# Optimization experiments

Measured on AMD Instinct MI355X. Metric: run time of the kernel, lower is better.

Reference implementation:

```python
import jax, jax.numpy as jnp
import numpy as np

N, T, D_FEAT, H = 8192, 60, 6, 64
NEG_SLOPE = 0.01  # torch LeakyReLU default


def setup_inputs() -> dict:
    key = jax.random.key(0)
    ks = jax.random.split(key, 20)
    s = lambda k, shape, fan: jax.random.normal(k, shape, jnp.float32) * (1.0 / np.sqrt(fan))
    inp = {
        'x': jax.random.normal(ks[0], (N, T, D_FEAT), jnp.float32),
        # LSTM layer 0 (input D_FEAT) and layer 1 (input H); gate order i,f,g,o
        'Wih0': s(ks[1], (4 * H, D_FEAT), H), 'Whh0': s(ks[2], (4 * H, H), H),
        'bih0': s(ks[3], (4 * H,), H), 'bhh0': s(ks[4], (4 * H,), H),
        'Wih1': s(ks[5], (4 * H, H), H), 'Whh1': s(ks[6], (4 * H, H), H),
        'bih1': s(ks[7], (4 * H,), H), 'bhh1': s(ks[8], (4 * H,), H),
        # GAT layer: transformation Linear(H,H) and attention vector a [2H,1] (randn in torch)
        'Wt': s(ks[9], (H, H), H), 'bt': s(ks[10], (H,), H),
        'a': jax.random.normal(ks[11], (2 * H, 1), jnp.float32),
        # fc and fc_out
        'Wfc': s(ks[12], (H, H), H), 'bfc': s(ks[13], (H,), H),
        'Wout': s(ks[14], (1, H), H), 'bout': s(ks[15], (1,), H),
    }
    return inp


def _lstm_layer(x, Wih, Whh, bih, bhh):
    # x: [N, T, Din] -> outputs [N, T, H]
    xg = jnp.einsum('ntd,gd->ntg', x, Wih) + bih + bhh  # precompute input gates

    def step(carry, xt):
        h, c = carry
        gates = xt + h @ Whh.T  # [N, 4H]
        i, f, g, o = jnp.split(gates, 4, axis=-1)
        c = jax.nn.sigmoid(f) * c + jax.nn.sigmoid(i) * jnp.tanh(g)
        h = jax.nn.sigmoid(o) * jnp.tanh(c)
        return (h, c), h

    n = x.shape[0]
    h0 = jnp.zeros((n, Whh.shape[1]), x.dtype)
    (_, _), hs = jax.lax.scan(step, (h0, h0), jnp.swapaxes(xg, 0, 1))
    return jnp.swapaxes(hs, 0, 1)


def _gat_layer(x, Wt, bt, a):
    # att[i,j] = leaky_relu(a1 . Wx_j + a2 . Wx_i); softmax over j; out = att @ x
    h = x @ Wt.T + bt                    # [N, H]
    hdim = h.shape[1]
    s1 = (h @ a[:hdim]).squeeze(-1)      # a1 . Wx_j  -> column term
    s2 = (h @ a[hdim:]).squeeze(-1)      # a2 . Wx_i  -> row term
    scores = jax.nn.leaky_relu(s2[:, None] + s1[None, :], NEG_SLOPE)  # [N, N]
    att = jax.nn.softmax(scores, axis=1)
    return att @ x


def reference(x, Wih0, Whh0, bih0, bhh0, Wih1, Whh1, bih1, bhh1,
              Wt, bt, a, Wfc, bfc, Wout, bout):
    out = _lstm_layer(x, Wih0, Whh0, bih0, bhh0)
    out = _lstm_layer(out, Wih1, Whh1, bih1, bhh1)
    last = out[:, -1, :]                 # [N, H]
    hidden = _gat_layer(last, Wt, bt, a) + last  # num_layers_gat = 1
    hidden = jax.nn.leaky_relu(hidden @ Wfc.T + bfc, NEG_SLOPE)
    return (hidden @ Wout.T + bout).squeeze(-1)  # [N]
```

## Files before the change

kernel.cpp:

```cpp
#include <hip/hip_runtime.h>

#define NN 8192
#define TT 60
#define DF 6
#define HH 64
#define GG 256
#define RS 132
#define CH 32
#define NB 256

typedef _Float16 half8 __attribute__((ext_vector_type(8)));
typedef float f32x4 __attribute__((ext_vector_type(4)));
#define MFMA16(a, b, c) __builtin_amdgcn_mfma_f32_16x16x32_f16((a), (b), (c), 0, 0, 0)

#define LOG2E 1.44269504f

__device__ __forceinline__ float lrelu_(float x) { return x > 0.0f ? x : 0.01f * x; }

__device__ __forceinline__ float lstm_act2(float gi, float gf, float gg, float go,
                                           float& c)
{
    const float ei = __builtin_amdgcn_exp2f(gi * -LOG2E);
    const float ef = __builtin_amdgcn_exp2f(gf * -LOG2E);
    const float eg = __builtin_amdgcn_exp2f(fminf(gg * (-2.f * LOG2E), 63.f));
    const float sf = __builtin_amdgcn_rcpf(1.f + ef);
    const float tg_si = (1.f - eg) * __builtin_amdgcn_rcpf((1.f + ei) * (1.f + eg));
    c = __builtin_fmaf(sf, c, tg_si);
    const float eo = __builtin_amdgcn_exp2f(go * -LOG2E);
    const float ec = __builtin_amdgcn_exp2f(fminf(c * (-2.f * LOG2E), 63.f));
    return (1.f - ec) * __builtin_amdgcn_rcpf((1.f + eo) * (1.f + ec));
}

__device__ __forceinline__ half8 ldw8(const float* __restrict__ p) {
    const float4* q = (const float4*)p;
    float4 u = q[0], v = q[1];
    half8 r;
    r[0]=(_Float16)u.x; r[1]=(_Float16)u.y; r[2]=(_Float16)u.z; r[3]=(_Float16)u.w;
    r[4]=(_Float16)v.x; r[5]=(_Float16)v.y; r[6]=(_Float16)v.z; r[7]=(_Float16)v.w;
    return r;
}

#define SXW (TT * 8 + 8)

__global__ __launch_bounds__(512, 4)
void lstm_fused_kernel(const float* __restrict__ x,
                       const float* __restrict__ Wih0, const float* __restrict__ Whh0,
                       const float* __restrict__ bih0, const float* __restrict__ bhh0,
                       const float* __restrict__ Wih1, const float* __restrict__ Whh1,
                       const float* __restrict__ bih1, const float* __restrict__ bhh1,
                       const float* __restrict__ Wt, const float* __restrict__ bt,
                       const float* __restrict__ av,
                       float* __restrict__ last_out,
                       float* __restrict__ s1g, float* __restrict__ s2g)
{
    __shared__ _Float16 sxp[16][SXW];
    __shared__ _Float16 h0buf[2][16][72];
    __shared__ _Float16 h1buf[2][16][72];
    __shared__ _Float16 zero16[8];
    __shared__ float sv1[HH], sv2[HH], sc12[2];

    const int tid  = threadIdx.x;
    const int w    = tid >> 6;
    const int grp  = w >> 2;
    const int cg   = w & 3;
    const int lane = tid & 63;
    const int quad = lane >> 4;
    const int l15  = lane & 15;
    const int hc   = cg * 16 + l15;
    const int n0   = blockIdx.x * 16;

    for (int i = tid; i < 16 * SXW / 2; i += 512) ((unsigned*)sxp)[i] = 0u;
    for (int i = tid; i < 2 * 16 * 72 / 2; i += 512) ((unsigned*)h0buf)[i] = 0u;
    for (int i = tid; i < 2 * 16 * 72 / 2; i += 512) ((unsigned*)h1buf)[i] = 0u;
    if (tid < 4) ((unsigned*)zero16)[tid] = 0u;
    __syncthreads();

    for (int idx = tid; idx < 16 * TT * DF; idx += 512) {
        const int m = idx / (TT * DF);
        const int r = idx - m * (TT * DF);
        const int t = r / DF;
        const int d = r - t * DF;
        sxp[m][t * 8 + d] = (_Float16)x[(size_t)(n0 + m) * (TT * DF) + r];
    }

    if (tid < HH) {
        float a1 = 0.f, a2 = 0.f;
        #pragma unroll 8
        for (int h = 0; h < HH; h++) {
            const float wt = Wt[h * HH + tid];
            a1 += wt * av[h];
            a2 += wt * av[HH + h];
        }
        sv1[tid] = a1; sv2[tid] = a2;
    } else if (tid == 64 || tid == 65) {
        const float* ap = av + (tid - 64) * HH;
        float c = 0.f;
        #pragma unroll 8
        for (int h = 0; h < HH; h++) c += bt[h] * ap[h];
        sc12[tid - 64] = c;
    }

    half8 wA[4][2], wB[4][2];
    float bias[4];
    half8 hzero;
    #pragma unroll
    for (int j = 0; j < 8; j++) hzero[j] = (_Float16)0.f;

    if (grp == 0) {
        #pragma unroll
        for (int nt = 0; nt < 4; nt++) {
            const int g = nt * 64 + hc;
            wA[nt][0] = ldw8(Whh0 + (size_t)g * HH + quad * 8);
            wA[nt][1] = ldw8(Whh0 + (size_t)g * HH + 32 + quad * 8);
            bias[nt]  = bih0[g] + bhh0[g];
            half8 t = hzero;
            if (quad == 0) {
                #pragma unroll
                for (int j = 0; j < DF; j++) t[j] = (_Float16)Wih0[g * DF + j];
            }
            wB[nt][0] = t;
            wB[nt][1] = hzero;
        }
    } else {
        #pragma unroll
        for (int nt = 0; nt < 4; nt++) {
            const int g = nt * 64 + hc;
            wA[nt][0] = ldw8(Wih1 + (size_t)g * HH + quad * 8);
            wA[nt][1] = ldw8(Wih1 + (size_t)g * HH + 32 + quad * 8);
            wB[nt][0] = ldw8(Whh1 + (size_t)g * HH + quad * 8);
            wB[nt][1] = ldw8(Whh1 + (size_t)g * HH + 32 + quad * 8);
            bias[nt]  = bih1[g] + bhh1[g];
        }
    }

    float cs[4] = {0.f, 0.f, 0.f, 0.f};
    __syncthreads();

    for (int i = 0; i <= TT; i++) {
        const int p = i & 1;
        if (grp == 0) {
            if (i < TT) {
                const half8 a0 = *(const half8*)&h0buf[p][l15][quad * 8];
                const half8 a1 = *(const half8*)&h0buf[p][l15][32 + quad * 8];
                const _Float16* xap = (quad == 0) ? &sxp[l15][i * 8] : zero16;
                const half8 ax = *(const half8*)xap;
                f32x4 gv[4];
                #pragma unroll
                for (int nt = 0; nt < 4; nt++) {
                    f32x4 c; c[0] = bias[nt]; c[1] = bias[nt]; c[2] = bias[nt]; c[3] = bias[nt];
                    c = MFMA16(ax, wB[nt][0], c);
                    c = MFMA16(a0, wA[nt][0], c);
                    c = MFMA16(a1, wA[nt][1], c);
                    gv[nt] = c;
                }
                _Float16 (*h0w)[72] = h0buf[p ^ 1];
                #pragma unroll
                for (int reg = 0; reg < 4; reg++) {
                    const float hv = lstm_act2(gv[0][reg], gv[1][reg], gv[2][reg], gv[3][reg], cs[reg]);
                    h0w[quad * 4 + reg][hc] = (_Float16)hv;
                }
            }
        } else {
            if (i > 0) {
                const half8 a00 = *(const half8*)&h0buf[p][l15][quad * 8];
                const half8 a01 = *(const half8*)&h0buf[p][l15][32 + quad * 8];
                const half8 a10 = *(const half8*)&h1buf[p][l15][quad * 8];
                const half8 a11 = *(const half8*)&h1buf[p][l15][32 + quad * 8];
                f32x4 gv[4];
                #pragma unroll
                for (int nt = 0; nt < 4; nt++) {
                    f32x4 c; c[0] = bias[nt]; c[1] = bias[nt]; c[2] = bias[nt]; c[3] = bias[nt];
                    c = MFMA16(a00, wA[nt][0], c);
                    c = MFMA16(a01, wA[nt][1], c);
                    c = MFMA16(a10, wB[nt][0], c);
                    c = MFMA16(a11, wB[nt][1], c);
                    gv[nt] = c;
                }
                _Float16 (*h1w)[72] = h1buf[p ^ 1];
                #pragma unroll
                for (int reg = 0; reg < 4; reg++) {
                    const float hv = lstm_act2(gv[0][reg], gv[1][reg], gv[2][reg], gv[3][reg], cs[reg]);
                    h1w[quad * 4 + reg][hc] = (_Float16)hv;
                    if (i == TT) last_out[(size_t)(n0 + quad * 4 + reg) * HH + hc] = hv;
                }
            }
        }
        __syncthreads();
    }

    {
        const _Float16 (*hf)[72] = h1buf[1];
        const int r  = tid >> 5;
        const int c0 = tid & 31;
        const float h1a = (float)hf[r][c0];
        const float h1b = (float)hf[r][c0 + 32];
        float p1 = h1a * sv1[c0] + h1b * sv1[c0 + 32];
        float p2 = h1a * sv2[c0] + h1b * sv2[c0 + 32];
        #pragma unroll
        for (int off = 16; off > 0; off >>= 1) {
            p1 += __shfl_xor(p1, off);
            p2 += __shfl_xor(p2, off);
        }
        if (c0 == 0) {
            s1g[n0 + r] = p1 + sc12[0];
            s2g[n0 + r] = p2 + sc12[1];
        }
    }
}

__global__ __launch_bounds__(256)
void rankfac_kernel(const float* __restrict__ s1g, const float* __restrict__ s2g,
                    float* __restrict__ Z, float* __restrict__ Ai, float* __restrict__ Bi,
                    float* __restrict__ U, float* __restrict__ W,
                    int* __restrict__ iperm, float* __restrict__ sortedD)
{
    __shared__ float sb[NN];
    __shared__ float sred[256];
    __shared__ int   sRank[32];
    const int tid = threadIdx.x;
    const int b   = blockIdx.x;
    const int j0  = b * 32;

    for (int idx = tid; idx < NN; idx += 256) sb[idx] = s1g[idx];
    if (tid < 32) sRank[tid] = 0;
    __syncthreads();

    float m = -1e30f;
    for (int idx = tid; idx < NN; idx += 256) m = fmaxf(m, sb[idx]);
    sred[tid] = m;
    __syncthreads();
    for (int s = 128; s > 0; s >>= 1) {
        if (tid < s) sred[tid] = fmaxf(sred[tid], sred[tid + s]);
        __syncthreads();
    }
    const float s1max = sred[0];

    if (tid < 32) {
        const int j = j0 + tid;
        const float z  = s2g[j] + s1max;
        const float mi = lrelu_(z);
        Z[j]  = z;
        Ai[j] = __expf(z - mi);
        Bi[j] = __expf(0.01f * z - mi);
        const float d = sb[j] - s1max;
        U[j] = __expf(d);
        W[j] = __expf(0.01f * d);
    }
    {
        const int jl = tid & 31;
        const int part = tid >> 5;
        const float sj = sb[j0 + jl];
        const int jg = j0 + jl;
        int cnt = 0;
        const int k0 = part * (NN / 8);
        #pragma unroll 4
        for (int k = k0; k < k0 + NN / 8; k++) {
            const float sk = sb[k];
            cnt += (sk < sj || (sk == sj && k < jg)) ? 1 : 0;
        }
        atomicAdd(&sRank[jl], cnt);
    }
    __syncthreads();
    if (tid < 32) {
        const int r = sRank[tid];
        iperm[r] = j0 + tid;
        sortedD[r] = sb[j0 + tid] - s1max;
    }
}

__global__ __launch_bounds__(256)
void scanA_kernel(const float* __restrict__ last, const float* __restrict__ U,
                  const float* __restrict__ W, const int* __restrict__ iperm,
                  float* __restrict__ chunkSum)
{
    __shared__ int   sj[CH];
    __shared__ float su[CH], sw[CH];
    __shared__ float al[CH][HH], bl[CH][HH];
    const int tid = threadIdx.x;
    const int b   = blockIdx.x;
    if (tid < CH) {
        const int j = iperm[b * CH + tid];
        sj[tid] = j; su[tid] = U[j]; sw[tid] = W[j];
    }
    __syncthreads();
    for (int idx = tid; idx < CH * HH; idx += 256) {
        const int rr = idx >> 6, c = idx & 63;
        const float lv = last[(size_t)sj[rr] * HH + c];
        al[rr][c] = su[rr] * lv;
        bl[rr][c] = sw[rr] * lv;
    }
    __syncthreads();
    if (tid < 130) {
        const int c = tid;
        float s = 0.f;
        if (c < 64) {
            for (int rr = 0; rr < CH; rr++) s += al[rr][c];
        } else if (c < 128) {
            for (int rr = 0; rr < CH; rr++) s += bl[rr][c - 64];
        } else if (c == 128) {
            for (int rr = 0; rr < CH; rr++) s += su[rr];
        } else {
            for (int rr = 0; rr < CH; rr++) s += sw[rr];
        }
        chunkSum[b * RS + c] = s;
    }
}

__global__ __launch_bounds__(256)
void scanB_kernel(const float* __restrict__ chunkSum, float* __restrict__ chunkOfs)
{
    __shared__ float wt[4];
    const int c   = blockIdx.x;
    const bool rev = (c < 64) || (c == 128);
    const int tid = threadIdx.x;
    const int lane = tid & 63, wv = tid >> 6;
    const int idx = rev ? (NB - 1 - tid) : tid;
    const float orig = chunkSum[idx * RS + c];
    float v = orig;
    #pragma unroll
    for (int d = 1; d < 64; d <<= 1) {
        const float t = __shfl_up(v, d);
        if (lane >= d) v += t;
    }
    if (lane == 63) wt[wv] = v;
    __syncthreads();
    float off = 0.f;
    for (int q = 0; q < wv; q++) off += wt[q];
    chunkOfs[idx * RS + c] = v + off - orig;
}

__global__ __launch_bounds__(256)
void scanC_kernel(const float* __restrict__ last, const float* __restrict__ U,
                  const float* __restrict__ W, const int* __restrict__ iperm,
                  const float* __restrict__ chunkOfs, float* __restrict__ PP)
{
    __shared__ int   sj[CH];
    __shared__ float su[CH], sw[CH];
    __shared__ float al[CH][HH], bl[CH][HH];
    const int tid = threadIdx.x;
    const int b   = blockIdx.x;
    if (tid < CH) {
        const int j = iperm[b * CH + tid];
        sj[tid] = j; su[tid] = U[j]; sw[tid] = W[j];
    }
    __syncthreads();
    for (int idx = tid; idx < CH * HH; idx += 256) {
        const int rr = idx >> 6, c = idx & 63;
        const float lv = last[(size_t)sj[rr] * HH + c];
        al[rr][c] = su[rr] * lv;
        bl[rr][c] = sw[rr] * lv;
    }
    __syncthreads();
    if (tid < 130) {
        const int c = tid;
        const bool rev = (c < 64) || (c == 128);
        float run = chunkOfs[b * RS + c];
        if (rev) {
            if (b == NB - 1) PP[(size_t)NN * RS + c] = 0.f;
            for (int rr = CH - 1; rr >= 0; rr--) {
                const float val = (c < 64) ? al[rr][c] : su[rr];
                run += val;
                PP[(size_t)(b * CH + rr) * RS + c] = run;
            }
        } else {
            for (int rr = 0; rr < CH; rr++) {
                PP[(size_t)(b * CH + rr) * RS + c] = run;
                run += (c < 128) ? bl[rr][c - 64] : sw[rr];
            }
            if (b == NB - 1) PP[(size_t)NN * RS + c] = run;
        }
    }
}

__global__ __launch_bounds__(256)
void applyfc_kernel(const float* __restrict__ last,
                    const float* __restrict__ Z, const float* __restrict__ Ai, const float* __restrict__ Bi,
                    const float* __restrict__ sortedD, const float* __restrict__ PP,
                    const float* __restrict__ Wfc, const float* __restrict__ bfc,
                    const float* __restrict__ Wout, const float* __restrict__ bout,
                    float* __restrict__ out)
{
    __shared__ float sdD[NN];
    __shared__ float sW[HH][HH + 1];
    __shared__ float sbF[HH], saF[HH];
    const int tid = threadIdx.x;
    for (int idx = tid; idx < NN; idx += 256) sdD[idx] = sortedD[idx];
    for (int idx = tid; idx < HH * HH; idx += 256) {
        const int h = idx >> 6, d = idx & 63;
        sW[d][h] = Wfc[idx];
    }
    if (tid < HH) { sbF[tid] = bfc[tid]; saF[tid] = Wout[tid]; }
    __syncthreads();

    const int wv = tid >> 6, lane = tid & 63;
    const int i0 = blockIdx.x * 32 + wv * 8;
    float zi[8]; int lo[8], hi[8];
    #pragma unroll
    for (int q = 0; q < 8; q++) { zi[q] = Z[i0 + q]; lo[q] = 0; hi[q] = NN; }
    for (int iter = 0; iter < 13; iter++) {
        #pragma unroll
        for (int q = 0; q < 8; q++) {
            if (lo[q] < hi[q]) {
                const int mid = (lo[q] + hi[q]) >> 1;
                const float dm = sdD[mid];
                if (zi[q] + dm > 0.f) hi[q] = mid; else lo[q] = mid + 1;
            }
        }
    }
    float gv[8];
    #pragma unroll
    for (int q = 0; q < 8; q++) {
        const int i = i0 + q;
        const float* rowp = PP + (size_t)lo[q] * RS;
        const float pu  = rowp[lane];
        const float pw  = rowp[64 + lane];
        const float pud = rowp[128];
        const float pwd = rowp[129];
        const float ai = Ai[i], bi = Bi[i];
        const float numer = bi * pw + ai * pu;
        const float den   = bi * pwd + ai * pud;
        const float lv = last[(size_t)i * HH + lane];
        gv[q] = numer * __builtin_amdgcn_rcpf(den) + lv;
    }
    const float bo = bout[0];
    #pragma unroll
    for (int q = 0; q < 8; q++) {
        float acc = sbF[lane];
        #pragma unroll
        for (int d = 0; d < HH; d++) acc += __shfl(gv[q], d) * sW[d][lane];
        float prod = lrelu_(acc) * saF[lane];
        #pragma unroll
        for (int off = 32; off > 0; off >>= 1) prod += __shfl_xor(prod, off);
        if (lane == 0) out[i0 + q] = prod + bo;
    }
}

extern "C" void kernel_launch(void* const* d_in, const int* in_sizes, int n_in,
                              void* d_out, int out_size, void* d_ws, size_t ws_size,
                              hipStream_t stream)
{
    (void)in_sizes; (void)n_in; (void)out_size; (void)ws_size;
    const float* x    = (const float*)d_in[0];
    const float* Wih0 = (const float*)d_in[1];
    const float* Whh0 = (const float*)d_in[2];
    const float* bih0 = (const float*)d_in[3];
    const float* bhh0 = (const float*)d_in[4];
    const float* Wih1 = (const float*)d_in[5];
    const float* Whh1 = (const float*)d_in[6];
    const float* bih1 = (const float*)d_in[7];
    const float* bhh1 = (const float*)d_in[8];
    const float* Wt   = (const float*)d_in[9];
    const float* bt   = (const float*)d_in[10];
    const float* a    = (const float*)d_in[11];
    const float* Wfc  = (const float*)d_in[12];
    const float* bfc  = (const float*)d_in[13];
    const float* Wout = (const float*)d_in[14];
    const float* bout = (const float*)d_in[15];
    float* out = (float*)d_out;

    float* ws       = (float*)d_ws;
    float* last     = ws;
    float* s1g      = last + (size_t)NN*HH;
    float* s2g      = s1g + NN;
    float* Z        = s2g + NN;
    float* Ai       = Z + NN;
    float* Bi       = Ai + NN;
    float* U        = Bi + NN;
    float* W        = U + NN;
    float* sortedD  = W + NN;
    int*   iperm    = (int*)(sortedD + NN);
    float* chunkSum = (float*)(iperm + NN);
    float* chunkOfs = chunkSum + NB*RS;
    float* PP       = chunkOfs + NB*RS;

    lstm_fused_kernel<<<dim3(NN / 16), dim3(512), 0, stream>>>(
        x, Wih0, Whh0, bih0, bhh0, Wih1, Whh1, bih1, bhh1,
        Wt, bt, a, last, s1g, s2g);
    rankfac_kernel<<<dim3(NB), dim3(256), 0, stream>>>(
        s1g, s2g, Z, Ai, Bi, U, W, iperm, sortedD);
    scanA_kernel<<<dim3(NB), dim3(256), 0, stream>>>(last, U, W, iperm, chunkSum);
    scanB_kernel<<<dim3(130), dim3(256), 0, stream>>>(chunkSum, chunkOfs);
    scanC_kernel<<<dim3(NB), dim3(256), 0, stream>>>(last, U, W, iperm, chunkOfs, PP);
    applyfc_kernel<<<dim3(NB), dim3(256), 0, stream>>>(
        last, Z, Ai, Bi, sortedD, PP, Wfc, bfc, Wout, bout, out);
}
```

Before: 258.9 us.

## Split LSTM gate work across 16 waves with LDS gate exchange

The fused LSTM kernel doubles its block size to 1024 threads. Each wave now computes two of the four gate tiles per layer and writes the gate pre-activations to a shared-memory buffer. After a barrier, all threads apply the activations, each handling two sequence rows, so the transcendental work is spread over twice as many lanes. The cost is an extra __syncthreads per timestep, LDS round-trips for the gate values and a larger shared-memory footprint, with fewer resident blocks per CU in exchange for more waves per block.

```diff
diff --git a/kernel.cpp b/kernel.cpp
--- a/kernel.cpp
+++ b/kernel.cpp
@@ -10,6 +10,7 @@
 #define NB 256
 
 typedef _Float16 half8 __attribute__((ext_vector_type(8)));
+typedef _Float16 half2v __attribute__((ext_vector_type(2)));
 typedef float f32x4 __attribute__((ext_vector_type(4)));
 #define MFMA16(a, b, c) __builtin_amdgcn_mfma_f32_16x16x32_f16((a), (b), (c), 0, 0, 0)
 
@@ -42,7 +43,7 @@
 
 #define SXW (TT * 8 + 8)
 
-__global__ __launch_bounds__(512, 4)
+__global__ __launch_bounds__(1024, 8)
 void lstm_fused_kernel(const float* __restrict__ x,
                        const float* __restrict__ Wih0, const float* __restrict__ Whh0,
                        const float* __restrict__ bih0, const float* __restrict__ bhh0,
@@ -56,26 +57,32 @@
     __shared__ _Float16 sxp[16][SXW];
     __shared__ _Float16 h0buf[2][16][72];
     __shared__ _Float16 h1buf[2][16][72];
+    __shared__ float    gbuf[2][16][65][4];
     __shared__ _Float16 zero16[8];
     __shared__ float sv1[HH], sv2[HH], sc12[2];
 
     const int tid  = threadIdx.x;
     const int w    = tid >> 6;
-    const int grp  = w >> 2;
-    const int cg   = w & 3;
+    const int lyr  = w >> 3;
+    const int sub  = w & 7;
+    const int cg   = sub >> 1;
+    const int gh   = sub & 1;
     const int lane = tid & 63;
     const int quad = lane >> 4;
     const int l15  = lane & 15;
     const int hc   = cg * 16 + l15;
     const int n0   = blockIdx.x * 16;
-
-    for (int i = tid; i < 16 * SXW / 2; i += 512) ((unsigned*)sxp)[i] = 0u;
-    for (int i = tid; i < 2 * 16 * 72 / 2; i += 512) ((unsigned*)h0buf)[i] = 0u;
-    for (int i = tid; i < 2 * 16 * 72 / 2; i += 512) ((unsigned*)h1buf)[i] = 0u;
+    const int seqA0 = sub;
+    const int seqA1 = sub + 8;
+    const int colA  = lane;
+
+    for (int i = tid; i < 16 * SXW / 2; i += 1024) ((unsigned*)sxp)[i] = 0u;
+    for (int i = tid; i < 2 * 16 * 72 / 2; i += 1024) ((unsigned*)h0buf)[i] = 0u;
+    for (int i = tid; i < 2 * 16 * 72 / 2; i += 1024) ((unsigned*)h1buf)[i] = 0u;
     if (tid < 4) ((unsigned*)zero16)[tid] = 0u;
     __syncthreads();
 
-    for (int idx = tid; idx < 16 * TT * DF; idx += 512) {
+    for (int idx = tid; idx < 16 * TT * DF; idx += 1024) {
         const int m = idx / (TT * DF);
         const int r = idx - m * (TT * DF);
         const int t = r / DF;
@@ -100,95 +107,108 @@
         sc12[tid - 64] = c;
     }
 
-    half8 wA[4][2], wB[4][2];
-    float bias[4];
+    half8 wA[2][2], wB[2][2];
+    float bias[2];
     half8 hzero;
     #pragma unroll
     for (int j = 0; j < 8; j++) hzero[j] = (_Float16)0.f;
 
-    if (grp == 0) {
+    if (lyr == 0) {
         #pragma unroll
-        for (int nt = 0; nt < 4; nt++) {
-            const int g = nt * 64 + hc;
-            wA[nt][0] = ldw8(Whh0 + (size_t)g * HH + quad * 8);
-            wA[nt][1] = ldw8(Whh0 + (size_t)g * HH + 32 + quad * 8);
-            bias[nt]  = bih0[g] + bhh0[g];
+        for (int ln = 0; ln < 2; ln++) {
+            const int g = (gh * 2 + ln) * 64 + hc;
+            wA[ln][0] = ldw8(Whh0 + (size_t)g * HH + quad * 8);
+            wA[ln][1] = ldw8(Whh0 + (size_t)g * HH + 32 + quad * 8);
+            bias[ln]  = bih0[g] + bhh0[g];
             half8 t = hzero;
             if (quad == 0) {
                 #pragma unroll
                 for (int j = 0; j < DF; j++) t[j] = (_Float16)Wih0[g * DF + j];
             }
-            wB[nt][0] = t;
-            wB[nt][1] = hzero;
+            wB[ln][0] = t;
+            wB[ln][1] = hzero;
         }
     } else {
         #pragma unroll
-        for (int nt = 0; nt < 4; nt++) {
-            const int g = nt * 64 + hc;
-            wA[nt][0] = ldw8(Wih1 + (size_t)g * HH + quad * 8);
-            wA[nt][1] = ldw8(Wih1 + (size_t)g * HH + 32 + quad * 8);
-            wB[nt][0] = ldw8(Whh1 + (size_t)g * HH + quad * 8);
-            wB[nt][1] = ldw8(Whh1 + (size_t)g * HH + 32 + quad * 8);
-            bias[nt]  = bih1[g] + bhh1[g];
-        }
-    }
-
-    float cs[4] = {0.f, 0.f, 0.f, 0.f};
+        for (int ln = 0; ln < 2; ln++) {
+            const int g = (gh * 2 + ln) * 64 + hc;
+            wA[ln][0] = ldw8(Wih1 + (size_t)g * HH + quad * 8);
+            wA[ln][1] = ldw8(Wih1 + (size_t)g * HH + 32 + quad * 8);
+            wB[ln][0] = ldw8(Whh1 + (size_t)g * HH + quad * 8);
+            wB[ln][1] = ldw8(Whh1 + (size_t)g * HH + 32 + quad * 8);
+            bias[ln]  = bih1[g] + bhh1[g];
+        }
+    }
+
+    float cs0 = 0.f, cs1 = 0.f;
     __syncthreads();
 
     for (int i = 0; i <= TT; i++) {
         const int p = i & 1;
-        if (grp == 0) {
-            if (i < TT) {
+        const bool live = (lyr == 0) ? (i < TT) : (i > 0);
+
+        if (live) {
+            f32x4 gv0, gv1;
+            if (lyr == 0) {
                 const half8 a0 = *(const half8*)&h0buf[p][l15][quad * 8];
                 const half8 a1 = *(const half8*)&h0buf[p][l15][32 + quad * 8];
                 const _Float16* xap = (quad == 0) ? &sxp[l15][i * 8] : zero16;
                 const half8 ax = *(const half8*)xap;
-                f32x4 gv[4];
-                #pragma unroll
-                for (int nt = 0; nt < 4; nt++) {
-                    f32x4 c; c[0] = bias[nt]; c[1] = bias[nt]; c[2] = bias[nt]; c[3] = bias[nt];
-                    c = MFMA16(ax, wB[nt][0], c);
-                    c = MFMA16(a0, wA[nt][0], c);
-                    c = MFMA16(a1, wA[nt][1], c);
-                    gv[nt] = c;
-                }
-                _Float16 (*h0w)[72] = h0buf[p ^ 1];
-                #pragma unroll
-                for (int reg = 0; reg < 4; reg++) {
-                    const float hv = lstm_act2(gv[0][reg], gv[1][reg], gv[2][reg], gv[3][reg], cs[reg]);
-                    h0w[quad * 4 + reg][hc] = (_Float16)hv;
-                }
-            }
-        } else {
-            if (i > 0) {
+                f32x4 c0; c0[0] = bias[0]; c0[1] = bias[0]; c0[2] = bias[0]; c0[3] = bias[0];
+                c0 = MFMA16(ax, wB[0][0], c0);
+                c0 = MFMA16(a0, wA[0][0], c0);
+                c0 = MFMA16(a1, wA[0][1], c0);
+                f32x4 c1; c1[0] = bias[1]; c1[1] = bias[1]; c1[2] = bias[1]; c1[3] = bias[1];
+                c1 = MFMA16(ax, wB[1][0], c1);
+                c1 = MFMA16(a0, wA[1][0], c1);
+                c1 = MFMA16(a1, wA[1][1], c1);
+                gv0 = c0; gv1 = c1;
+            } else {
                 const half8 a00 = *(const half8*)&h0buf[p][l15][quad * 8];
                 const half8 a01 = *(const half8*)&h0buf[p][l15][32 + quad * 8];
                 const half8 a10 = *(const half8*)&h1buf[p][l15][quad * 8];
                 const half8 a11 = *(const half8*)&h1buf[p][l15][32 + quad * 8];
-                f32x4 gv[4];
-                #pragma unroll
-                for (int nt = 0; nt < 4; nt++) {
-                    f32x4 c; c[0] = bias[nt]; c[1] = bias[nt]; c[2] = bias[nt]; c[3] = bias[nt];
-                    c = MFMA16(a00, wA[nt][0], c);
-                    c = MFMA16(a01, wA[nt][1], c);
-                    c = MFMA16(a10, wB[nt][0], c);
-                    c = MFMA16(a11, wB[nt][1], c);
-                    gv[nt] = c;
+                f32x4 c0; c0[0] = bias[0]; c0[1] = bias[0]; c0[2] = bias[0]; c0[3] = bias[0];
+                c0 = MFMA16(a00, wA[0][0], c0);
+                c0 = MFMA16(a01, wA[0][1], c0);
+                c0 = MFMA16(a10, wB[0][0], c0);
+                c0 = MFMA16(a11, wB[0][1], c0);
+                f32x4 c1; c1[0] = bias[1]; c1[1] = bias[1]; c1[2] = bias[1]; c1[3] = bias[1];
+                c1 = MFMA16(a00, wA[1][0], c1);
+                c1 = MFMA16(a01, wA[1][1], c1);
+                c1 = MFMA16(a10, wB[1][0], c1);
+                c1 = MFMA16(a11, wB[1][1], c1);
+                gv0 = c0; gv1 = c1;
+            }
+            #pragma unroll
+            for (int reg = 0; reg < 4; reg++) {
+                float2 t; t.x = gv0[reg]; t.y = gv1[reg];
+                *(float2*)&gbuf[lyr][quad * 4 + reg][hc][gh * 2] = t;
+            }
+        }
+        __syncthreads();
+
+        if (live) {
+            const float4 g0 = *(const float4*)&gbuf[lyr][seqA0][colA][0];
+            const float4 g1 = *(const float4*)&gbuf[lyr][seqA1][colA][0];
+            const float hv0 = lstm_act2(g0.x, g0.y, g0.z, g0.w, cs0);
+            const float hv1 = lstm_act2(g1.x, g1.y, g1.z, g1.w, cs1);
+            if (lyr == 0) {
+                h0buf[p ^ 1][seqA0][colA] = (_Float16)hv0;
+                h0buf[p ^ 1][seqA1][colA] = (_Float16)hv1;
+            } else {
+                h1buf[p ^ 1][seqA0][colA] = (_Float16)hv0;
+                h1buf[p ^ 1][seqA1][colA] = (_Float16)hv1;
+                if (i == TT) {
+                    last_out[(size_t)(n0 + seqA0) * HH + colA] = hv0;
+                    last_out[(size_t)(n0 + seqA1) * HH + colA] = hv1;
                 }
-                _Float16 (*h1w)[72] = h1buf[p ^ 1];
-                #pragma unroll
-                for (int reg = 0; reg < 4; reg++) {
-                    const float hv = lstm_act2(gv[0][reg], gv[1][reg], gv[2][reg], gv[3][reg], cs[reg]);
-                    h1w[quad * 4 + reg][hc] = (_Float16)hv;
-                    if (i == TT) last_out[(size_t)(n0 + quad * 4 + reg) * HH + hc] = hv;
-                }
             }
         }
         __syncthreads();
     }
 
-    {
+    if (tid < 512) {
         const _Float16 (*hf)[72] = h1buf[1];
         const int r  = tid >> 5;
         const int c0 = tid & 31;
@@ -473,7 +493,7 @@
     float* chunkOfs = chunkSum + NB*RS;
     float* PP       = chunkOfs + NB*RS;
 
-    lstm_fused_kernel<<<dim3(NN / 16), dim3(512), 0, stream>>>(
+    lstm_fused_kernel<<<dim3(NN / 16), dim3(1024), 0, stream>>>(
         x, Wih0, Whh0, bih0, bhh0, Wih1, Whh1, bih1, bhh1,
         Wt, bt, a, last, s1g, s2g);
     rankfac_kernel<<<dim3(NB), dim3(256), 0, stream>>>(
```

Measured after the change: 292.4 us. 13.0% more time.

## Fuse post-LSTM kernels into one cooperative kernel with grid syncs

Applied to the files above, without the earlier changes.

Merges the rank/factor, scan-A, scan-B, scan-C and apply-fc kernels into a single cooperative kernel that uses grid.sync between phases. This removes four kernel launches and their inter-kernel gaps. The separate chunk-offset scan kernel is dropped: each block now sums all preceding or following chunk sums serially, which is redundant O(NB) work per column. Cooperative launch needs all 256 blocks resident at once, and the merged shared-memory footprint is larger.

```diff
diff --git a/kernel.cpp b/kernel.cpp
--- a/kernel.cpp
+++ b/kernel.cpp
@@ -1,4 +1,7 @@
 #include <hip/hip_runtime.h>
+#include <hip/hip_cooperative_groups.h>
+
+namespace cg = cooperative_groups;
 
 #define NN 8192
 #define TT 60
@@ -209,14 +212,27 @@
 }
 
 __global__ __launch_bounds__(256)
-void rankfac_kernel(const float* __restrict__ s1g, const float* __restrict__ s2g,
-                    float* __restrict__ Z, float* __restrict__ Ai, float* __restrict__ Bi,
-                    float* __restrict__ U, float* __restrict__ W,
-                    int* __restrict__ iperm, float* __restrict__ sortedD)
+void post_kernel(const float* __restrict__ last,
+                 const float* __restrict__ s1g, const float* __restrict__ s2g,
+                 float* __restrict__ Z, float* __restrict__ Ai, float* __restrict__ Bi,
+                 float* __restrict__ U, float* __restrict__ W,
+                 int* __restrict__ iperm, float* __restrict__ sortedD,
+                 float* __restrict__ chunkSum, float* __restrict__ PP,
+                 const float* __restrict__ Wfc, const float* __restrict__ bfc,
+                 const float* __restrict__ Wout, const float* __restrict__ bout,
+                 float* __restrict__ out)
 {
+    cg::grid_group grid = cg::this_grid();
+
     __shared__ float sb[NN];
     __shared__ float sred[256];
     __shared__ int   sRank[32];
+    __shared__ int   sj[CH];
+    __shared__ float su[CH], sw[CH];
+    __shared__ float al[CH][HH], bl[CH][HH];
+    __shared__ float sW[HH][HH + 1];
+    __shared__ float sbF[HH], saF[HH];
+
     const int tid = threadIdx.x;
     const int b   = blockIdx.x;
     const int j0  = b * 32;
@@ -249,14 +265,14 @@
     {
         const int jl = tid & 31;
         const int part = tid >> 5;
-        const float sj = sb[j0 + jl];
+        const float sj_ = sb[j0 + jl];
         const int jg = j0 + jl;
         int cnt = 0;
         const int k0 = part * (NN / 8);
         #pragma unroll 4
         for (int k = k0; k < k0 + NN / 8; k++) {
             const float sk = sb[k];
-            cnt += (sk < sj || (sk == sj && k < jg)) ? 1 : 0;
+            cnt += (sk < sj_ || (sk == sj_ && k < jg)) ? 1 : 0;
         }
         atomicAdd(&sRank[jl], cnt);
     }
@@ -266,18 +282,9 @@
         iperm[r] = j0 + tid;
         sortedD[r] = sb[j0 + tid] - s1max;
     }
-}
-
-__global__ __launch_bounds__(256)
-void scanA_kernel(const float* __restrict__ last, const float* __restrict__ U,
-                  const float* __restrict__ W, const int* __restrict__ iperm,
-                  float* __restrict__ chunkSum)
-{
-    __shared__ int   sj[CH];
-    __shared__ float su[CH], sw[CH];
-    __shared__ float al[CH][HH], bl[CH][HH];
-    const int tid = threadIdx.x;
-    const int b   = blockIdx.x;
+
+    grid.sync();
+
     if (tid < CH) {
         const int j = iperm[b * CH + tid];
         sj[tid] = j; su[tid] = U[j]; sw[tid] = W[j];
@@ -304,58 +311,15 @@
         }
         chunkSum[b * RS + c] = s;
     }
-}
-
-__global__ __launch_bounds__(256)
-void scanB_kernel(const float* __restrict__ chunkSum, float* __restrict__ chunkOfs)
-{
-    __shared__ float wt[4];
-    const int c   = blockIdx.x;
-    const bool rev = (c < 64) || (c == 128);
-    const int tid = threadIdx.x;
-    const int lane = tid & 63, wv = tid >> 6;
-    const int idx = rev ? (NB - 1 - tid) : tid;
-    const float orig = chunkSum[idx * RS + c];
-    float v = orig;
-    #pragma unroll
-    for (int d = 1; d < 64; d <<= 1) {
-        const float t = __shfl_up(v, d);
-        if (lane >= d) v += t;
-    }
-    if (lane == 63) wt[wv] = v;
-    __syncthreads();
-    float off = 0.f;
-    for (int q = 0; q < wv; q++) off += wt[q];
-    chunkOfs[idx * RS + c] = v + off - orig;
-}
-
-__global__ __launch_bounds__(256)
-void scanC_kernel(const float* __restrict__ last, const float* __restrict__ U,
-                  const float* __restrict__ W, const int* __restrict__ iperm,
-                  const float* __restrict__ chunkOfs, float* __restrict__ PP)
-{
-    __shared__ int   sj[CH];
-    __shared__ float su[CH], sw[CH];
-    __shared__ float al[CH][HH], bl[CH][HH];
-    const int tid = threadIdx.x;
-    const int b   = blockIdx.x;
-    if (tid < CH) {
-        const int j = iperm[b * CH + tid];
-        sj[tid] = j; su[tid] = U[j]; sw[tid] = W[j];
-    }
-    __syncthreads();
-    for (int idx = tid; idx < CH * HH; idx += 256) {
-        const int rr = idx >> 6, c = idx & 63;
-        const float lv = last[(size_t)sj[rr] * HH + c];
-        al[rr][c] = su[rr] * lv;
-        bl[rr][c] = sw[rr] * lv;
-    }
-    __syncthreads();
+
+    grid.sync();
+
     if (tid < 130) {
         const int c = tid;
         const bool rev = (c < 64) || (c == 128);
-        float run = chunkOfs[b * RS + c];
+        float run = 0.f;
         if (rev) {
+            for (int k = NB - 1; k > b; k--) run += chunkSum[k * RS + c];
             if (b == NB - 1) PP[(size_t)NN * RS + c] = 0.f;
             for (int rr = CH - 1; rr >= 0; rr--) {
                 const float val = (c < 64) ? al[rr][c] : su[rr];
@@ -363,6 +327,7 @@
                 PP[(size_t)(b * CH + rr) * RS + c] = run;
             }
         } else {
+            for (int k = 0; k < b; k++) run += chunkSum[k * RS + c];
             for (int rr = 0; rr < CH; rr++) {
                 PP[(size_t)(b * CH + rr) * RS + c] = run;
                 run += (c < 128) ? bl[rr][c - 64] : sw[rr];
@@ -370,21 +335,10 @@
             if (b == NB - 1) PP[(size_t)NN * RS + c] = run;
         }
     }
-}
-
-__global__ __launch_bounds__(256)
-void applyfc_kernel(const float* __restrict__ last,
-                    const float* __restrict__ Z, const float* __restrict__ Ai, const float* __restrict__ Bi,
-                    const float* __restrict__ sortedD, const float* __restrict__ PP,
-                    const float* __restrict__ Wfc, const float* __restrict__ bfc,
-                    const float* __restrict__ Wout, const float* __restrict__ bout,
-                    float* __restrict__ out)
-{
-    __shared__ float sdD[NN];
-    __shared__ float sW[HH][HH + 1];
-    __shared__ float sbF[HH], saF[HH];
-    const int tid = threadIdx.x;
-    for (int idx = tid; idx < NN; idx += 256) sdD[idx] = sortedD[idx];
+
+    grid.sync();
+
+    for (int idx = tid; idx < NN; idx += 256) sb[idx] = sortedD[idx];
     for (int idx = tid; idx < HH * HH; idx += 256) {
         const int h = idx >> 6, d = idx & 63;
         sW[d][h] = Wfc[idx];
@@ -393,7 +347,7 @@
     __syncthreads();
 
     const int wv = tid >> 6, lane = tid & 63;
-    const int i0 = blockIdx.x * 32 + wv * 8;
+    const int i0 = b * 32 + wv * 8;
     float zi[8]; int lo[8], hi[8];
     #pragma unroll
     for (int q = 0; q < 8; q++) { zi[q] = Z[i0 + q]; lo[q] = 0; hi[q] = NN; }
@@ -402,7 +356,7 @@
         for (int q = 0; q < 8; q++) {
             if (lo[q] < hi[q]) {
                 const int mid = (lo[q] + hi[q]) >> 1;
-                const float dm = sdD[mid];
+                const float dm = sb[mid];
                 if (zi[q] + dm > 0.f) hi[q] = mid; else lo[q] = mid + 1;
             }
         }
@@ -476,11 +430,13 @@
     lstm_fused_kernel<<<dim3(NN / 16), dim3(512), 0, stream>>>(
         x, Wih0, Whh0, bih0, bhh0, Wih1, Whh1, bih1, bhh1,
         Wt, bt, a, last, s1g, s2g);
-    rankfac_kernel<<<dim3(NB), dim3(256), 0, stream>>>(
-        s1g, s2g, Z, Ai, Bi, U, W, iperm, sortedD);
-    scanA_kernel<<<dim3(NB), dim3(256), 0, stream>>>(last, U, W, iperm, chunkSum);
-    scanB_kernel<<<dim3(130), dim3(256), 0, stream>>>(chunkSum, chunkOfs);
-    scanC_kernel<<<dim3(NB), dim3(256), 0, stream>>>(last, U, W, iperm, chunkOfs, PP);
-    applyfc_kernel<<<dim3(NB), dim3(256), 0, stream>>>(
-        last, Z, Ai, Bi, sortedD, PP, Wfc, bfc, Wout, bout, out);
+
+    void* args[] = {
+        (void*)&last, (void*)&s1g, (void*)&s2g,
+        (void*)&Z, (void*)&Ai, (void*)&Bi, (void*)&U, (void*)&W,
+        (void*)&iperm, (void*)&sortedD, (void*)&chunkSum, (void*)&PP,
+        (void*)&Wfc, (void*)&bfc, (void*)&Wout, (void*)&bout, (void*)&out
+    };
+    hipLaunchCooperativeKernel(reinterpret_cast<void*>(post_kernel),
+                               dim3(NB), dim3(256), args, 0, stream);
 }
```

Result: slower. 414.5 us (+60.1%).

## Widen rank/apply blocks, drop scanB by recomputing chunk offsets in scanC

Applied to the files above, without the earlier changes.

The rank kernel now runs 1024 threads per block, uses a wave-shuffle max reduction and float4 LDS reads in the rank-counting loop. The separate scanB launch is removed: each scanC thread sums the other chunks' totals directly, which trades one launch and a sync point for redundant global reads. applyfc now uses 512 threads with 4 rows per wave instead of 8, giving more parallelism for the binary search and FC stage. The LSTM kernel still dominates total time, so the tail-stage gains may be small.

```diff
diff --git a/kernel.cpp b/kernel.cpp
--- a/kernel.cpp
+++ b/kernel.cpp
@@ -208,32 +208,39 @@
     }
 }
 
-__global__ __launch_bounds__(256)
+__global__ __launch_bounds__(1024)
 void rankfac_kernel(const float* __restrict__ s1g, const float* __restrict__ s2g,
                     float* __restrict__ Z, float* __restrict__ Ai, float* __restrict__ Bi,
                     float* __restrict__ U, float* __restrict__ W,
                     int* __restrict__ iperm, float* __restrict__ sortedD)
 {
     __shared__ float sb[NN];
-    __shared__ float sred[256];
+    __shared__ float sredw[16];
     __shared__ int   sRank[32];
-    const int tid = threadIdx.x;
-    const int b   = blockIdx.x;
-    const int j0  = b * 32;
-
-    for (int idx = tid; idx < NN; idx += 256) sb[idx] = s1g[idx];
+    const int tid  = threadIdx.x;
+    const int lane = tid & 63;
+    const int wv   = tid >> 6;
+    const int b    = blockIdx.x;
+    const int j0   = b * 32;
+
+    for (int idx = tid; idx < NN; idx += 1024) sb[idx] = s1g[idx];
     if (tid < 32) sRank[tid] = 0;
     __syncthreads();
 
     float m = -1e30f;
-    for (int idx = tid; idx < NN; idx += 256) m = fmaxf(m, sb[idx]);
-    sred[tid] = m;
-    __syncthreads();
-    for (int s = 128; s > 0; s >>= 1) {
-        if (tid < s) sred[tid] = fmaxf(sred[tid], sred[tid + s]);
-        __syncthreads();
-    }
-    const float s1max = sred[0];
+    for (int idx = tid; idx < NN; idx += 1024) m = fmaxf(m, sb[idx]);
+    #pragma unroll
+    for (int off = 32; off > 0; off >>= 1) m = fmaxf(m, __shfl_xor(m, off));
+    if (lane == 0) sredw[wv] = m;
+    __syncthreads();
+    if (tid == 0) {
+        float mm = sredw[0];
+        #pragma unroll
+        for (int q = 1; q < 16; q++) mm = fmaxf(mm, sredw[q]);
+        sredw[0] = mm;
+    }
+    __syncthreads();
+    const float s1max = sredw[0];
 
     if (tid < 32) {
         const int j = j0 + tid;
@@ -251,12 +258,17 @@
         const int part = tid >> 5;
         const float sj = sb[j0 + jl];
         const int jg = j0 + jl;
+        const int k0 = part * (NN / 32);
+        const float4* sb4 = (const float4*)&sb[k0];
         int cnt = 0;
-        const int k0 = part * (NN / 8);
-        #pragma unroll 4
-        for (int k = k0; k < k0 + NN / 8; k++) {
-            const float sk = sb[k];
-            cnt += (sk < sj || (sk == sj && k < jg)) ? 1 : 0;
+        #pragma unroll 8
+        for (int it = 0; it < NN / 32 / 4; it++) {
+            const float4 v = sb4[it];
+            const int kb = k0 + it * 4;
+            cnt += (v.x < sj || (v.x == sj && kb + 0 < jg)) ? 1 : 0;
+            cnt += (v.y < sj || (v.y == sj && kb + 1 < jg)) ? 1 : 0;
+            cnt += (v.z < sj || (v.z == sj && kb + 2 < jg)) ? 1 : 0;
+            cnt += (v.w < sj || (v.w == sj && kb + 3 < jg)) ? 1 : 0;
         }
         atomicAdd(&sRank[jl], cnt);
     }
@@ -307,32 +319,9 @@
 }
 
 __global__ __launch_bounds__(256)
-void scanB_kernel(const float* __restrict__ chunkSum, float* __restrict__ chunkOfs)
-{
-    __shared__ float wt[4];
-    const int c   = blockIdx.x;
-    const bool rev = (c < 64) || (c == 128);
-    const int tid = threadIdx.x;
-    const int lane = tid & 63, wv = tid >> 6;
-    const int idx = rev ? (NB - 1 - tid) : tid;
-    const float orig = chunkSum[idx * RS + c];
-    float v = orig;
-    #pragma unroll
-    for (int d = 1; d < 64; d <<= 1) {
-        const float t = __shfl_up(v, d);
-        if (lane >= d) v += t;
-    }
-    if (lane == 63) wt[wv] = v;
-    __syncthreads();
-    float off = 0.f;
-    for (int q = 0; q < wv; q++) off += wt[q];
-    chunkOfs[idx * RS + c] = v + off - orig;
-}
-
-__global__ __launch_bounds__(256)
 void scanC_kernel(const float* __restrict__ last, const float* __restrict__ U,
                   const float* __restrict__ W, const int* __restrict__ iperm,
-                  const float* __restrict__ chunkOfs, float* __restrict__ PP)
+                  const float* __restrict__ chunkSum, float* __restrict__ PP)
 {
     __shared__ int   sj[CH];
     __shared__ float su[CH], sw[CH];
@@ -354,8 +343,11 @@
     if (tid < 130) {
         const int c = tid;
         const bool rev = (c < 64) || (c == 128);
-        float run = chunkOfs[b * RS + c];
+        float run = 0.f;
         if (rev) {
+            #pragma unroll 8
+            for (int k = 0; k < NB; k++)
+                run += (k > b) ? chunkSum[k * RS + c] : 0.f;
             if (b == NB - 1) PP[(size_t)NN * RS + c] = 0.f;
             for (int rr = CH - 1; rr >= 0; rr--) {
                 const float val = (c < 64) ? al[rr][c] : su[rr];
@@ -363,6 +355,9 @@
                 PP[(size_t)(b * CH + rr) * RS + c] = run;
             }
         } else {
+            #pragma unroll 8
+            for (int k = 0; k < NB; k++)
+                run += (k < b) ? chunkSum[k * RS + c] : 0.f;
             for (int rr = 0; rr < CH; rr++) {
                 PP[(size_t)(b * CH + rr) * RS + c] = run;
                 run += (c < 128) ? bl[rr][c - 64] : sw[rr];
@@ -372,7 +367,7 @@
     }
 }
 
-__global__ __launch_bounds__(256)
+__global__ __launch_bounds__(512)
 void applyfc_kernel(const float* __restrict__ last,
                     const float* __restrict__ Z, const float* __restrict__ Ai, const float* __restrict__ Bi,
                     const float* __restrict__ sortedD, const float* __restrict__ PP,
@@ -384,8 +379,8 @@
     __shared__ float sW[HH][HH + 1];
     __shared__ float sbF[HH], saF[HH];
     const int tid = threadIdx.x;
-    for (int idx = tid; idx < NN; idx += 256) sdD[idx] = sortedD[idx];
-    for (int idx = tid; idx < HH * HH; idx += 256) {
+    for (int idx = tid; idx < NN; idx += 512) sdD[idx] = sortedD[idx];
+    for (int idx = tid; idx < HH * HH; idx += 512) {
         const int h = idx >> 6, d = idx & 63;
         sW[d][h] = Wfc[idx];
     }
@@ -393,13 +388,13 @@
     __syncthreads();
 
     const int wv = tid >> 6, lane = tid & 63;
-    const int i0 = blockIdx.x * 32 + wv * 8;
-    float zi[8]; int lo[8], hi[8];
+    const int i0 = blockIdx.x * 32 + wv * 4;
+    float zi[4]; int lo[4], hi[4];
     #pragma unroll
-    for (int q = 0; q < 8; q++) { zi[q] = Z[i0 + q]; lo[q] = 0; hi[q] = NN; }
+    for (int q = 0; q < 4; q++) { zi[q] = Z[i0 + q]; lo[q] = 0; hi[q] = NN; }
     for (int iter = 0; iter < 13; iter++) {
         #pragma unroll
-        for (int q = 0; q < 8; q++) {
+        for (int q = 0; q < 4; q++) {
             if (lo[q] < hi[q]) {
                 const int mid = (lo[q] + hi[q]) >> 1;
                 const float dm = sdD[mid];
@@ -407,9 +402,9 @@
             }
         }
     }
-    float gv[8];
+    float gv[4];
     #pragma unroll
-    for (int q = 0; q < 8; q++) {
+    for (int q = 0; q < 4; q++) {
         const int i = i0 + q;
         const float* rowp = PP + (size_t)lo[q] * RS;
         const float pu  = rowp[lane];
@@ -424,7 +419,7 @@
     }
     const float bo = bout[0];
     #pragma unroll
-    for (int q = 0; q < 8; q++) {
+    for (int q = 0; q < 4; q++) {
         float acc = sbF[lane];
         #pragma unroll
         for (int d = 0; d < HH; d++) acc += __shfl(gv[q], d) * sW[d][lane];
@@ -476,11 +471,10 @@
     lstm_fused_kernel<<<dim3(NN / 16), dim3(512), 0, stream>>>(
         x, Wih0, Whh0, bih0, bhh0, Wih1, Whh1, bih1, bhh1,
         Wt, bt, a, last, s1g, s2g);
-    rankfac_kernel<<<dim3(NB), dim3(256), 0, stream>>>(
+    rankfac_kernel<<<dim3(NB), dim3(1024), 0, stream>>>(
         s1g, s2g, Z, Ai, Bi, U, W, iperm, sortedD);
     scanA_kernel<<<dim3(NB), dim3(256), 0, stream>>>(last, U, W, iperm, chunkSum);
-    scanB_kernel<<<dim3(130), dim3(256), 0, stream>>>(chunkSum, chunkOfs);
-    scanC_kernel<<<dim3(NB), dim3(256), 0, stream>>>(last, U, W, iperm, chunkOfs, PP);
-    applyfc_kernel<<<dim3(NB), dim3(256), 0, stream>>>(
+    scanC_kernel<<<dim3(NB), dim3(256), 0, stream>>>(last, U, W, iperm, chunkSum, PP);
+    applyfc_kernel<<<dim3(NB), dim3(512), 0, stream>>>(
         last, Z, Ai, Bi, sortedD, PP, Wfc, bfc, Wout, bout, out);
 }
```

Result: faster. 243.5 us (-6.0%).
